# Optimization experiments

Hardware: AMD Instinct MI355X
Metric: run time of the kernel (lower is better)

The kernel has to match this reference:

```python
import jax, jax.numpy as jnp
import numpy as np

B, T, IN, H, L = 64, 512, 512, 512, 2


def setup_inputs() -> dict:
    key = jax.random.key(0)
    ks = jax.random.split(key, 7)
    s_ih = 1.0 / np.sqrt(H)
    x = jax.random.normal(ks[0], (B, T, IN), dtype=jnp.float32)
    encoder_h = jax.random.normal(ks[1], (L, B, H), dtype=jnp.float32)
    # stacked GRUCell params per layer (input_size == hidden_size so stackable)
    W_ih = jax.random.uniform(ks[2], (L, 3 * H, IN), jnp.float32, -s_ih, s_ih)
    W_hh = jax.random.uniform(ks[3], (L, 3 * H, H), jnp.float32, -s_ih, s_ih)
    b_ih = jax.random.uniform(ks[4], (L, 3 * H), jnp.float32, -s_ih, s_ih)
    b_hh = jax.random.uniform(ks[5], (L, 3 * H), jnp.float32, -s_ih, s_ih)
    return {"x": x, "encoder_h": encoder_h, "W_ih": W_ih, "W_hh": W_hh,
            "b_ih": b_ih, "b_hh": b_hh}


def _gru_cell(x, h, W_ih, W_hh, b_ih, b_hh):
    # torch.nn.GRUCell math
    gi = x @ W_ih.T + b_ih            # [B, 3H]
    gh = h @ W_hh.T + b_hh            # [B, 3H]
    i_r, i_z, i_n = jnp.split(gi, 3, axis=-1)
    h_r, h_z, h_n = jnp.split(gh, 3, axis=-1)
    r = jax.nn.sigmoid(i_r + h_r)
    z = jax.nn.sigmoid(i_z + h_z)
    n = jnp.tanh(i_n + r * h_n)
    return (1.0 - z) * n + z * h


def reference(x, encoder_h, W_ih, W_hh, b_ih, b_hh):
    num_layers = W_ih.shape[0]

    def step(h_carry, x_t):
        hs = []
        inp = x_t
        for j in range(num_layers):  # small static layer loop
            h_new = _gru_cell(inp, h_carry[j], W_ih[j], W_hh[j], b_ih[j], b_hh[j])
            hs.append(h_new)
            inp = h_new
        return tuple(hs), inp

    h0 = tuple(encoder_h[j] for j in range(num_layers))
    xs = jnp.swapaxes(x, 0, 1)                 # [T, B, IN]
    h_final, outs = jax.lax.scan(step, h0, xs)  # outs: [T, B, H]
    out = jnp.swapaxes(outs, 0, 1)             # [B, T, H]
    h = jnp.stack(h_final, axis=0)             # [L, B, H]
    return out, h
```

## Files before the change

kernel.cpp:

```cpp
#include <hip/hip_runtime.h>


#define NBLK 256
#define NTHR 512
#define Bsz  64
#define Tlen 512
#define Kd   512
#define Hd   512
#define KC   64
#define LP   67

__device__ __forceinline__ float sigf(float v){ return 1.0f/(1.0f+__expf(-v)); }
__device__ __forceinline__ float tanhx(float v){
  float e=__expf(-2.0f*fabsf(v)); float t=(1.0f-e)/(1.0f+e); return v<0.0f?-t:t;
}
__device__ __forceinline__ unsigned umin2(unsigned a, unsigned b){ return a<b?a:b; }

__device__ __forceinline__ void st_coh(float* p, float v){
  asm volatile("global_store_dword %0, %1, off sc0 sc1" :: "v"(p), "v"(v) : "memory");
}
__device__ __forceinline__ void st_coh_u(unsigned* p, unsigned v){
  asm volatile("global_store_dword %0, %1, off sc0 sc1" :: "v"(p), "v"(v) : "memory");
}
__device__ __forceinline__ void wait_vm0(){ asm volatile("s_waitcnt vmcnt(0)" ::: "memory"); }

__device__ __forceinline__ void grid_barrier(unsigned* slots, unsigned target, int tid){
  wait_vm0();
  __syncthreads();
  if(tid == 0) st_coh_u(slots + blockIdx.x, target);
  if(tid < 64){
    const unsigned* p0 = slots + tid;
    for(;;){
      unsigned a,b,c,d;
      asm volatile(
        "global_load_dword %0, %4, off sc0 sc1\n\t"
        "global_load_dword %1, %5, off sc0 sc1\n\t"
        "global_load_dword %2, %6, off sc0 sc1\n\t"
        "global_load_dword %3, %7, off sc0 sc1\n\t"
        "s_waitcnt vmcnt(0)"
        : "=v"(a),"=v"(b),"=v"(c),"=v"(d)
        : "v"(p0), "v"(p0+64), "v"(p0+128), "v"(p0+192)
        : "memory");
      unsigned m = umin2(umin2(a,b), umin2(c,d));
      #pragma unroll
      for(int off=32; off; off>>=1)
        m = umin2(m, (unsigned)__shfl_xor((int)m, off, 64));
      if(m >= target) break;
      __builtin_amdgcn_s_sleep(1);
    }
  }
  __syncthreads();
  __builtin_amdgcn_fence(__ATOMIC_ACQUIRE, "agent");
}

__device__ __forceinline__ void stageA(float* sbuf, const float* __restrict__ x,
                                       int t, int ch, int tid){
  #pragma unroll
  for(int it=0; it<2; ++it){
    int q  = it*NTHR + tid;
    int b  = q >> 4;
    int k4 = (q & 15) << 2;
    const float4 v = *(const float4*)(x + ((size_t)b*Tlen + t)*Kd + ch*KC + k4);
    sbuf[(k4+0)*LP + b] = v.x;
    sbuf[(k4+1)*LP + b] = v.y;
    sbuf[(k4+2)*LP + b] = v.z;
    sbuf[(k4+3)*LP + b] = v.w;
  }
}

extern "C" __global__ void __launch_bounds__(NTHR, 2)
gru_persist(const float* __restrict__ x,
            const float* __restrict__ eh,
            const float* __restrict__ Wih,
            const float* __restrict__ Whh,
            const float* __restrict__ bih,
            const float* __restrict__ bhh,
            float* __restrict__ out,
            float* __restrict__ ws)
{
  __shared__ float smem[2*KC*LP];

  unsigned* slots = (unsigned*)ws;
  float* h0T = ws + 256;
  float* h1T = h0T + 2*Kd*Bsz;
  float* htail = out + (size_t)Bsz*Tlen*Hd;

  const int tid  = threadIdx.x;
  const int lane = tid & 63;
  const int wv   = __builtin_amdgcn_readfirstlane(tid >> 6);
  const int cell = blockIdx.x >> 7;
  const int cb   = blockIdx.x & 127;
  const int col0 = cb * 4;
  unsigned bar = 1;

  {
    int i = blockIdx.x*NTHR + tid;
    if(i < 2*Kd*Bsz){
      int l = i >> 15, k = (i >> 6) & 511, b = i & 63;
      float v = eh[(size_t)(l*Bsz + b)*Hd + k];
      st_coh((l ? h1T : h0T) + Kd*Bsz + k*Bsz + b, v);
    }
  }
  grid_barrier(slots, bar, tid); bar++;

  const float* WiB = Wih + (size_t)cell*3*Hd*Kd + (size_t)col0*Kd;
  const float* WhB = Whh + (size_t)cell*3*Hd*Kd + (size_t)col0*Kd;
  const int ec = wv & 3;
  const int ecol = col0 + ec;
  const float bi0 = bih[cell*1536 + 0*Hd + ecol] + bhh[cell*1536 + 0*Hd + ecol];
  const float bi1 = bih[cell*1536 + 1*Hd + ecol] + bhh[cell*1536 + 1*Hd + ecol];
  const float bi2 = bih[cell*1536 + 2*Hd + ecol];
  const float bh2 = bhh[cell*1536 + 2*Hd + ecol];

  for(int t = 0; t <= Tlen; ++t){
    const bool active = (cell == 0) ? (t < Tlen) : (t >= 1);
    if(active){
      const int s = (cell == 0) ? t : (t - 1);
      float* hbase = (cell == 0) ? h0T : h1T;
      const float* hprev = hbase + ((s+1)&1)*Kd*Bsz;
      float*       hout  = hbase + (s&1)*Kd*Bsz;
      const float* inT   = h0T + (s&1)*Kd*Bsz;

      float pr[4]={0,0,0,0}, pz[4]={0,0,0,0}, pni[4]={0,0,0,0}, pnh[4]={0,0,0,0};

      if(cell == 0){
        stageA(smem, x, t, 0, tid);
        __syncthreads();
        for(int ch = 0; ch < 8; ++ch){
          const float* cur = smem + (ch&1)*(KC*LP);
          if(ch < 7) stageA(smem + ((ch+1)&1)*(KC*LP), x, t, ch+1, tid);
          #pragma unroll
          for(int j = 0; j < 8; ++j){
            const int kl = (wv<<3) + j;
            const int kg = (ch<<6) + kl;
            const float xv = cur[kl*LP + lane];
            const float hv = hprev[kg*Bsz + lane];
            #pragma unroll
            for(int c = 0; c < 4; ++c){
              pr[c]  = fmaf(xv, WiB[(size_t)c*Kd + kg], pr[c]);
              pz[c]  = fmaf(xv, WiB[(size_t)Hd*Kd + c*Kd + kg], pz[c]);
              pni[c] = fmaf(xv, WiB[(size_t)2*Hd*Kd + c*Kd + kg], pni[c]);
              pr[c]  = fmaf(hv, WhB[(size_t)c*Kd + kg], pr[c]);
              pz[c]  = fmaf(hv, WhB[(size_t)Hd*Kd + c*Kd + kg], pz[c]);
              pnh[c] = fmaf(hv, WhB[(size_t)2*Hd*Kd + c*Kd + kg], pnh[c]);
            }
          }
          __syncthreads();
        }
      } else {
        #pragma unroll 8
        for(int j = 0; j < 64; ++j){
          const int kg = (wv<<6) + j;
          const float xv = inT[kg*Bsz + lane];
          const float hv = hprev[kg*Bsz + lane];
          #pragma unroll
          for(int c = 0; c < 4; ++c){
            pr[c]  = fmaf(xv, WiB[(size_t)c*Kd + kg], pr[c]);
            pz[c]  = fmaf(xv, WiB[(size_t)Hd*Kd + c*Kd + kg], pz[c]);
            pni[c] = fmaf(xv, WiB[(size_t)2*Hd*Kd + c*Kd + kg], pni[c]);
            pr[c]  = fmaf(hv, WhB[(size_t)c*Kd + kg], pr[c]);
            pz[c]  = fmaf(hv, WhB[(size_t)Hd*Kd + c*Kd + kg], pz[c]);
            pnh[c] = fmaf(hv, WhB[(size_t)2*Hd*Kd + c*Kd + kg], pnh[c]);
          }
        }
        __syncthreads();
      }

      float* red = smem;
      #pragma unroll
      for(int c = 0; c < 4; ++c){
        red[(((c<<2)+0)*8 + wv)*64 + lane] = pr[c];
        red[(((c<<2)+1)*8 + wv)*64 + lane] = pz[c];
        red[(((c<<2)+2)*8 + wv)*64 + lane] = pni[c];
        red[(((c<<2)+3)*8 + wv)*64 + lane] = pnh[c];
      }
      __syncthreads();
      if(wv < 4){
        const int c = wv;
        float spr=0.f, spz=0.f, spni=0.f, spnh=0.f;
        #pragma unroll
        for(int w = 0; w < 8; ++w){
          spr  += red[(((c<<2)+0)*8 + w)*64 + lane];
          spz  += red[(((c<<2)+1)*8 + w)*64 + lane];
          spni += red[(((c<<2)+2)*8 + w)*64 + lane];
          spnh += red[(((c<<2)+3)*8 + w)*64 + lane];
        }
        const int col = col0 + c;
        const float hkeep = hprev[col*Bsz + lane];
        const float r = sigf(spr + bi0);
        const float z = sigf(spz + bi1);
        const float n = tanhx(spni + bi2 + r*(spnh + bh2));
        const float hnew = (1.0f - z)*n + z*hkeep;
        st_coh(hout + col*Bsz + lane, hnew);
        if(cell == 1)
          out[((size_t)lane*Tlen + s)*Hd + col] = hnew;
      }
    }
    grid_barrier(slots, bar, tid); bar++;
  }

  {
    int i = blockIdx.x*NTHR + tid;
    if(i < 2*Kd*Bsz){
      int l = i >> 15, b = (i >> 9) & 63, c = i & 511;
      const float* src = (l ? h1T : h0T) + Kd*Bsz;
      htail[i] = src[c*Bsz + b];
    }
  }
}

extern "C" void kernel_launch(void* const* d_in, const int* in_sizes, int n_in,
                              void* d_out, int out_size, void* d_ws, size_t ws_size,
                              hipStream_t stream) {
  (void)in_sizes; (void)n_in; (void)out_size; (void)ws_size;
  const float* x   = (const float*)d_in[0];
  const float* eh  = (const float*)d_in[1];
  const float* Wih = (const float*)d_in[2];
  const float* Whh = (const float*)d_in[3];
  const float* bih = (const float*)d_in[4];
  const float* bhh = (const float*)d_in[5];
  float* out = (float*)d_out;
  float* ws  = (float*)d_ws;

  hipMemsetAsync(d_ws, 0, 1024, stream);

  void* args[] = {(void*)&x, (void*)&eh, (void*)&Wih, (void*)&Whh,
                  (void*)&bih, (void*)&bhh, (void*)&out, (void*)&ws};
  hipLaunchCooperativeKernel((const void*)gru_persist, dim3(NBLK), dim3(NTHR),
                             args, 0, stream);
}
```

Before: 19.82 ms.

## Vectorize weight loads, prefetch hidden state, use atomic system-scope coherence

Replaces the inline-asm coherent loads and stores with HIP system-scope relaxed atomics and switches the barrier's acquire fence to workgroup scope. Weight reads become float4 vector loads through a quadfma helper. Layer-0 hidden-state values are prefetched into double-buffered registers alongside the x staging. The reduction buffer gets its own shared array so one syncthreads can go, and the previous h is kept in a register instead of being reloaded. The aim is fewer load instructions and less barrier and fence overhead per timestep. The risk is that system-scope atomics or the weaker fence change cache behaviour or visibility across blocks.

```diff
diff --git a/kernel.cpp b/kernel.cpp
--- a/kernel.cpp
+++ b/kernel.cpp
@@ -16,31 +16,30 @@
 }
 __device__ __forceinline__ unsigned umin2(unsigned a, unsigned b){ return a<b?a:b; }
 
-__device__ __forceinline__ void st_coh(float* p, float v){
-  asm volatile("global_store_dword %0, %1, off sc0 sc1" :: "v"(p), "v"(v) : "memory");
-}
-__device__ __forceinline__ void st_coh_u(unsigned* p, unsigned v){
-  asm volatile("global_store_dword %0, %1, off sc0 sc1" :: "v"(p), "v"(v) : "memory");
-}
-__device__ __forceinline__ void wait_vm0(){ asm volatile("s_waitcnt vmcnt(0)" ::: "memory"); }
+__device__ __forceinline__ float ld_sys(const float* p){
+  return __hip_atomic_load(const_cast<float*>(p), __ATOMIC_RELAXED, __HIP_MEMORY_SCOPE_SYSTEM);
+}
+__device__ __forceinline__ void st_sys(float* p, float v){
+  __hip_atomic_store(p, v, __ATOMIC_RELAXED, __HIP_MEMORY_SCOPE_SYSTEM);
+}
+__device__ __forceinline__ unsigned ld_sys_u(const unsigned* p){
+  return __hip_atomic_load(const_cast<unsigned*>(p), __ATOMIC_RELAXED, __HIP_MEMORY_SCOPE_SYSTEM);
+}
+__device__ __forceinline__ void st_sys_u(unsigned* p, unsigned v){
+  __hip_atomic_store(p, v, __ATOMIC_RELAXED, __HIP_MEMORY_SCOPE_SYSTEM);
+}
 
 __device__ __forceinline__ void grid_barrier(unsigned* slots, unsigned target, int tid){
-  wait_vm0();
   __syncthreads();
-  if(tid == 0) st_coh_u(slots + blockIdx.x, target);
+  asm volatile("" ::: "memory");
+  if(tid == 0) st_sys_u(slots + blockIdx.x, target);
   if(tid < 64){
     const unsigned* p0 = slots + tid;
     for(;;){
-      unsigned a,b,c,d;
-      asm volatile(
-        "global_load_dword %0, %4, off sc0 sc1\n\t"
-        "global_load_dword %1, %5, off sc0 sc1\n\t"
-        "global_load_dword %2, %6, off sc0 sc1\n\t"
-        "global_load_dword %3, %7, off sc0 sc1\n\t"
-        "s_waitcnt vmcnt(0)"
-        : "=v"(a),"=v"(b),"=v"(c),"=v"(d)
-        : "v"(p0), "v"(p0+64), "v"(p0+128), "v"(p0+192)
-        : "memory");
+      unsigned a = ld_sys_u(p0);
+      unsigned b = ld_sys_u(p0 + 64);
+      unsigned c = ld_sys_u(p0 + 128);
+      unsigned d = ld_sys_u(p0 + 192);
       unsigned m = umin2(umin2(a,b), umin2(c,d));
       #pragma unroll
       for(int off=32; off; off>>=1)
@@ -49,8 +48,8 @@
       __builtin_amdgcn_s_sleep(1);
     }
   }
+  __builtin_amdgcn_fence(__ATOMIC_ACQUIRE, "workgroup");
   __syncthreads();
-  __builtin_amdgcn_fence(__ATOMIC_ACQUIRE, "agent");
 }
 
 __device__ __forceinline__ void stageA(float* sbuf, const float* __restrict__ x,
@@ -68,6 +67,27 @@
   }
 }
 
+__device__ __forceinline__ void quadfma(const float* __restrict__ WiB,
+                                        const float* __restrict__ WhB, int kg,
+                                        const float* xv, const float* hv,
+                                        float* pr, float* pz, float* pni, float* pnh){
+  #pragma unroll
+  for(int c = 0; c < 4; ++c){
+    const float4 a0 = *(const float4*)(WiB + (size_t)c*Kd + kg);
+    const float4 a1 = *(const float4*)(WiB + ((size_t)Hd + c)*Kd + kg);
+    const float4 a2 = *(const float4*)(WiB + ((size_t)2*Hd + c)*Kd + kg);
+    const float4 b0 = *(const float4*)(WhB + (size_t)c*Kd + kg);
+    const float4 b1 = *(const float4*)(WhB + ((size_t)Hd + c)*Kd + kg);
+    const float4 b2 = *(const float4*)(WhB + ((size_t)2*Hd + c)*Kd + kg);
+    pr[c]  = fmaf(xv[0],a0.x, fmaf(xv[1],a0.y, fmaf(xv[2],a0.z, fmaf(xv[3],a0.w, pr[c]))));
+    pz[c]  = fmaf(xv[0],a1.x, fmaf(xv[1],a1.y, fmaf(xv[2],a1.z, fmaf(xv[3],a1.w, pz[c]))));
+    pni[c] = fmaf(xv[0],a2.x, fmaf(xv[1],a2.y, fmaf(xv[2],a2.z, fmaf(xv[3],a2.w, pni[c]))));
+    pr[c]  = fmaf(hv[0],b0.x, fmaf(hv[1],b0.y, fmaf(hv[2],b0.z, fmaf(hv[3],b0.w, pr[c]))));
+    pz[c]  = fmaf(hv[0],b1.x, fmaf(hv[1],b1.y, fmaf(hv[2],b1.z, fmaf(hv[3],b1.w, pz[c]))));
+    pnh[c] = fmaf(hv[0],b2.x, fmaf(hv[1],b2.y, fmaf(hv[2],b2.z, fmaf(hv[3],b2.w, pnh[c]))));
+  }
+}
+
 extern "C" __global__ void __launch_bounds__(NTHR, 2)
 gru_persist(const float* __restrict__ x,
             const float* __restrict__ eh,
@@ -78,7 +98,8 @@
             float* __restrict__ out,
             float* __restrict__ ws)
 {
-  __shared__ float smem[2*KC*LP];
+  __shared__ float sstage[2*KC*LP];
+  __shared__ float red[16*8*64];
 
   unsigned* slots = (unsigned*)ws;
   float* h0T = ws + 256;
@@ -98,19 +119,21 @@
     if(i < 2*Kd*Bsz){
       int l = i >> 15, k = (i >> 6) & 511, b = i & 63;
       float v = eh[(size_t)(l*Bsz + b)*Hd + k];
-      st_coh((l ? h1T : h0T) + Kd*Bsz + k*Bsz + b, v);
+      st_sys((l ? h1T : h0T) + Kd*Bsz + k*Bsz + b, v);
     }
   }
   grid_barrier(slots, bar, tid); bar++;
 
   const float* WiB = Wih + (size_t)cell*3*Hd*Kd + (size_t)col0*Kd;
   const float* WhB = Whh + (size_t)cell*3*Hd*Kd + (size_t)col0*Kd;
-  const int ec = wv & 3;
+  const int ec   = wv & 3;
   const int ecol = col0 + ec;
   const float bi0 = bih[cell*1536 + 0*Hd + ecol] + bhh[cell*1536 + 0*Hd + ecol];
   const float bi1 = bih[cell*1536 + 1*Hd + ecol] + bhh[cell*1536 + 1*Hd + ecol];
   const float bi2 = bih[cell*1536 + 2*Hd + ecol];
   const float bh2 = bhh[cell*1536 + 2*Hd + ecol];
+
+  float hkeep = eh[((size_t)(cell*Bsz) + lane)*Hd + ecol];
 
   for(int t = 0; t <= Tlen; ++t){
     const bool active = (cell == 0) ? (t < Tlen) : (t >= 1);
@@ -124,49 +147,41 @@
       float pr[4]={0,0,0,0}, pz[4]={0,0,0,0}, pni[4]={0,0,0,0}, pnh[4]={0,0,0,0};
 
       if(cell == 0){
-        stageA(smem, x, t, 0, tid);
+        float hvb[2][8];
+        #pragma unroll
+        for(int j=0;j<8;++j) hvb[0][j] = ld_sys(hprev + ((wv<<3)+j)*Bsz + lane);
+        stageA(sstage, x, t, 0, tid);
         __syncthreads();
+        #pragma unroll
         for(int ch = 0; ch < 8; ++ch){
-          const float* cur = smem + (ch&1)*(KC*LP);
-          if(ch < 7) stageA(smem + ((ch+1)&1)*(KC*LP), x, t, ch+1, tid);
+          const float* cur = sstage + (ch&1)*(KC*LP);
+          if(ch < 7){
+            stageA(sstage + ((ch+1)&1)*(KC*LP), x, t, ch+1, tid);
+            #pragma unroll
+            for(int j=0;j<8;++j)
+              hvb[(ch+1)&1][j] = ld_sys(hprev + (((ch+1)<<6)+(wv<<3)+j)*Bsz + lane);
+          }
+          float xv[8];
           #pragma unroll
-          for(int j = 0; j < 8; ++j){
-            const int kl = (wv<<3) + j;
-            const int kg = (ch<<6) + kl;
-            const float xv = cur[kl*LP + lane];
-            const float hv = hprev[kg*Bsz + lane];
-            #pragma unroll
-            for(int c = 0; c < 4; ++c){
-              pr[c]  = fmaf(xv, WiB[(size_t)c*Kd + kg], pr[c]);
-              pz[c]  = fmaf(xv, WiB[(size_t)Hd*Kd + c*Kd + kg], pz[c]);
-              pni[c] = fmaf(xv, WiB[(size_t)2*Hd*Kd + c*Kd + kg], pni[c]);
-              pr[c]  = fmaf(hv, WhB[(size_t)c*Kd + kg], pr[c]);
-              pz[c]  = fmaf(hv, WhB[(size_t)Hd*Kd + c*Kd + kg], pz[c]);
-              pnh[c] = fmaf(hv, WhB[(size_t)2*Hd*Kd + c*Kd + kg], pnh[c]);
-            }
-          }
+          for(int j=0;j<8;++j) xv[j] = cur[((wv<<3)+j)*LP + lane];
+          quadfma(WiB, WhB, (ch<<6)+(wv<<3),     &xv[0], &hvb[ch&1][0], pr,pz,pni,pnh);
+          quadfma(WiB, WhB, (ch<<6)+(wv<<3)+4,   &xv[4], &hvb[ch&1][4], pr,pz,pni,pnh);
           __syncthreads();
         }
       } else {
-        #pragma unroll 8
-        for(int j = 0; j < 64; ++j){
-          const int kg = (wv<<6) + j;
-          const float xv = inT[kg*Bsz + lane];
-          const float hv = hprev[kg*Bsz + lane];
+        #pragma unroll
+        for(int jq = 0; jq < 16; ++jq){
+          const int kg = (wv<<6) + (jq<<2);
+          float xv[4], hv[4];
           #pragma unroll
-          for(int c = 0; c < 4; ++c){
-            pr[c]  = fmaf(xv, WiB[(size_t)c*Kd + kg], pr[c]);
-            pz[c]  = fmaf(xv, WiB[(size_t)Hd*Kd + c*Kd + kg], pz[c]);
-            pni[c] = fmaf(xv, WiB[(size_t)2*Hd*Kd + c*Kd + kg], pni[c]);
-            pr[c]  = fmaf(hv, WhB[(size_t)c*Kd + kg], pr[c]);
-            pz[c]  = fmaf(hv, WhB[(size_t)Hd*Kd + c*Kd + kg], pz[c]);
-            pnh[c] = fmaf(hv, WhB[(size_t)2*Hd*Kd + c*Kd + kg], pnh[c]);
+          for(int u=0;u<4;++u){
+            xv[u] = ld_sys(inT   + (size_t)(kg+u)*Bsz + lane);
+            hv[u] = ld_sys(hprev + (size_t)(kg+u)*Bsz + lane);
           }
+          quadfma(WiB, WhB, kg, xv, hv, pr,pz,pni,pnh);
         }
-        __syncthreads();
       }
 
-      float* red = smem;
       #pragma unroll
       for(int c = 0; c < 4; ++c){
         red[(((c<<2)+0)*8 + wv)*64 + lane] = pr[c];
@@ -186,12 +201,12 @@
           spnh += red[(((c<<2)+3)*8 + w)*64 + lane];
         }
         const int col = col0 + c;
-        const float hkeep = hprev[col*Bsz + lane];
         const float r = sigf(spr + bi0);
         const float z = sigf(spz + bi1);
         const float n = tanhx(spni + bi2 + r*(spnh + bh2));
         const float hnew = (1.0f - z)*n + z*hkeep;
-        st_coh(hout + col*Bsz + lane, hnew);
+        hkeep = hnew;
+        st_sys(hout + col*Bsz + lane, hnew);
         if(cell == 1)
           out[((size_t)lane*Tlen + s)*Hd + col] = hnew;
       }
@@ -204,7 +219,7 @@
     if(i < 2*Kd*Bsz){
       int l = i >> 15, b = (i >> 9) & 63, c = i & 511;
       const float* src = (l ? h1T : h0T) + Kd*Bsz;
-      htail[i] = src[c*Bsz + b];
+      htail[i] = ld_sys(src + c*Bsz + b);
     }
   }
 }
```

New measurement: 68.31 ms. 3.45x slower.
